# Kernel tuning notes

Measured on AMD Instinct MI355X. Metric: run time of the kernel, lower is better.

Reference implementation:

```python
import jax, jax.numpy as jnp
import numpy as np

CAPACITY_FACTOR = 1.0
MIN_CAPACITY = 4


def setup_inputs() -> dict:
    key = jax.random.key(0)
    ks = jax.random.split(key, 4)
    B, S, D, E, F = 4, 2048, 1024, 16, 4096
    hidden_states = jax.random.normal(ks[0], (B, S, D), dtype=jnp.float32)
    wg = jax.random.normal(ks[1], (D, E), dtype=jnp.float32) * 0.02
    w1 = jax.random.normal(ks[2], (E, D, F), dtype=jnp.float32) * (1.0 / np.sqrt(D))
    b1 = jnp.zeros((E, F), dtype=jnp.float32)
    w2 = jax.random.normal(ks[3], (E, F, D), dtype=jnp.float32) * (1.0 / np.sqrt(F))
    b2 = jnp.zeros((E, D), dtype=jnp.float32)
    return {"hidden_states": hidden_states, "wg": wg, "w1": w1, "b1": b1, "w2": w2, "b2": b2}


def reference(hidden_states, wg, w1, b1, w2, b2):
    B, S, D = hidden_states.shape
    x = hidden_states.reshape(-1, D)                      # [T, D] tokens
    T = x.shape[0]
    E = wg.shape[1]
    capacity = max(int(np.ceil(T / E * CAPACITY_FACTOR)), MIN_CAPACITY)  # static

    # ---- TopKGate (k=1, no noise, no RTS) ----
    logits = x @ wg                                       # [T, E]
    gates = jax.nn.softmax(logits, axis=-1)
    idx1 = jnp.argmax(gates, axis=1)                      # [T]
    mask1 = jax.nn.one_hot(idx1, E, dtype=gates.dtype)    # [T, E]
    exp_counts = jnp.sum(mask1, axis=0).astype(jnp.int32) # per-expert token counts

    # load-balancing aux loss
    me = jnp.mean(gates, axis=0)
    ce = jnp.mean(mask1, axis=0)
    l_aux = jnp.sum(me * ce) * E

    # slot assignment within each expert, drop overflow tokens
    locations1 = jnp.cumsum(mask1, axis=0) - 1.0          # [T, E]
    mask1 = mask1 * (locations1 < capacity).astype(gates.dtype)
    locations1_s = jnp.sum(locations1 * mask1, axis=1).astype(jnp.int32)  # [T]
    gates1 = gates * mask1                                # [T, E] gate prob of kept assignment

    loc_oh = jax.nn.one_hot(locations1_s, capacity, dtype=gates.dtype)    # [T, C]
    combine = jnp.einsum('te,tc->tec', gates1, loc_oh)    # [T, E, C]
    dispatch = (combine > 0).astype(x.dtype)              # [T, E, C]

    # ---- dispatch -> grouped expert FFN -> combine ----
    disp = jnp.einsum('tec,td->ecd', dispatch, x)         # [E, C, D]
    h = jax.nn.gelu(jnp.einsum('ecd,edf->ecf', disp, w1) + b1[:, None, :])
    eo = jnp.einsum('ecf,efd->ecd', h, w2) + b2[:, None, :]  # [E, C, D]
    out = jnp.einsum('tec,ecd->td', combine, eo).reshape(B, S, D)
    return out, l_aux, exp_counts
```

## Files before the change

### kernel.cpp

```cpp
#include <hip/hip_runtime.h>

typedef unsigned short u16;
typedef unsigned int   u32;
typedef unsigned long long u64;
typedef __attribute__((ext_vector_type(8))) __bf16 bf16x8;
typedef __attribute__((ext_vector_type(4))) float  f32x4;

#define TOK 8192
#define DIM 1024
#define NE  16
#define NF  4096
#define CAP 512

__device__ __forceinline__ u16 f2bf(float f) {
    u32 u = __float_as_uint(f);
    u32 r = (u + 0x7FFFu + ((u >> 16) & 1u)) >> 16;
    return (u16)r;
}

__device__ __forceinline__ float gelu_tanh(float x) {
    float u = 0.7978845608028654f * (x + 0.044715f * x * x * x);
    float t = __expf(-2.f * fabsf(u));
    float th = (1.f - t) / (1.f + t);
    th = (u < 0.f) ? -th : th;
    return 0.5f * x * (1.f + th);
}

__device__ __forceinline__ void gld16(const void* g, void* l) {
    __builtin_amdgcn_global_load_lds(
        (const __attribute__((address_space(1))) void*)g,
        (__attribute__((address_space(3))) void*)l, 16, 0, 0);
}

__global__ void moe_init(float* me_sums) {
    if (threadIdx.x < NE) me_sums[threadIdx.x] = 0.f;
}

__global__ void moe_wgT(const float* __restrict__ wg, float* __restrict__ wgT) {
    int i = blockIdx.x * 256 + threadIdx.x;
    int d = i >> 4, e = i & 15;
    wgT[(size_t)e * DIM + d] = wg[i];
}

__global__ void moe_gate(const float* __restrict__ x, const float* __restrict__ wgT,
                         int* __restrict__ eidx, float* __restrict__ gp,
                         float* __restrict__ me_sums) {
    __shared__ float lme[NE];
    const int tid = threadIdx.x;
    if (tid < NE) lme[tid] = 0.f;
    __syncthreads();
    const int tok = blockIdx.x * 16 + (tid >> 4);
    const int e   = tid & 15;
    const float4* xp = (const float4*)(x + (size_t)tok * DIM);
    const float4* wp = (const float4*)(wgT + (size_t)e * DIM);
    float acc = 0.f;
#pragma unroll 4
    for (int i = 0; i < DIM / 4; ++i) {
        float4 a = xp[i], b = wp[i];
        acc = fmaf(a.x, b.x, acc); acc = fmaf(a.y, b.y, acc);
        acc = fmaf(a.z, b.z, acc); acc = fmaf(a.w, b.w, acc);
    }
    float mx = acc;
    for (int off = 8; off; off >>= 1) mx = fmaxf(mx, __shfl_xor(mx, off, 16));
    float ex = __expf(acc - mx);
    float sum = ex;
    for (int off = 8; off; off >>= 1) sum += __shfl_xor(sum, off, 16);
    float p = ex / sum;
    atomicAdd(&lme[e], p);
    float bv = acc; int bi = e;
    for (int off = 8; off; off >>= 1) {
        float ov = __shfl_xor(bv, off, 16);
        int   oi = __shfl_xor(bi, off, 16);
        if (ov > bv || (ov == bv && oi < bi)) { bv = ov; bi = oi; }
    }
    float pw = __shfl(p, bi, 16);
    if (e == 0) { eidx[tok] = bi; gp[tok] = pw; }
    __syncthreads();
    if (tid < 16) atomicAdd(&me_sums[tid], lme[tid]);
}

__global__ void moe_scan(const int* __restrict__ eidx, const float* __restrict__ me_sums,
                         int* __restrict__ slot, int* __restrict__ tos,
                         float* __restrict__ tail ) {
    __shared__ int wcnt[16][16];
    __shared__ int base[16];
    const int tid = threadIdx.x, wid = tid >> 6, lane = tid & 63;
    if (tid < 16) base[tid] = 0;
    for (int i = tid; i < NE * CAP; i += 1024) tos[i] = -1;
    __syncthreads();
    const u64 below = ((u64)1 << lane) - 1;
    for (int chunk = 0; chunk < TOK / 1024; ++chunk) {
        int t = chunk * 1024 + tid;
        int e = eidx[t];
        int rank = 0;
#pragma unroll
        for (int ex = 0; ex < 16; ++ex) {
            u64 m = __ballot(e == ex);
            if (e == ex)    rank = __popcll(m & below);
            if (lane == ex) wcnt[wid][ex] = __popcll(m);
        }
        __syncthreads();
        int pre = base[e];
        for (int w = 0; w < wid; ++w) pre += wcnt[w][e];
        int s = pre + rank;
        slot[t] = s;
        if (s < CAP) tos[e * CAP + s] = t;
        __syncthreads();
        if (tid < 16) {
            int tot = 0;
            for (int w = 0; w < 16; ++w) tot += wcnt[w][tid];
            base[tid] += tot;
        }
        __syncthreads();
    }
    if (tid == 0) {
        float laux = 0.f;
        for (int e2 = 0; e2 < 16; ++e2) {
            float me = me_sums[e2] / (float)TOK;
            float ce = (float)base[e2] / (float)TOK;
            laux += me * ce;
        }
        tail[0] = laux * (float)NE;
    }
    if (tid < 16) tail[1 + tid] = (float)base[tid];
}

__global__ void moe_gather(const float* __restrict__ x, const int* __restrict__ tos,
                           u16* __restrict__ Xg) {
    const int s = blockIdx.x, tid = threadIdx.x;
    const int t = tos[s];
    float4 v = make_float4(0.f, 0.f, 0.f, 0.f);
    if (t >= 0) v = *(const float4*)(x + (size_t)t * DIM + tid * 4);
    u32 lo = (u32)f2bf(v.x) | ((u32)f2bf(v.y) << 16);
    u32 hi = (u32)f2bf(v.z) | ((u32)f2bf(v.w) << 16);
    *(uint2*)(Xg + (size_t)s * DIM + tid * 4) = make_uint2(lo, hi);
}

__global__ void moe_zero_dropped(const int* __restrict__ slot, float* __restrict__ out) {
    const int t = blockIdx.x;
    if (slot[t] < CAP) return;
    *(float4*)(out + (size_t)t * DIM + threadIdx.x * 4) = make_float4(0.f, 0.f, 0.f, 0.f);
}

__global__ void moe_convT(const float* __restrict__ src, u16* __restrict__ dst,
                          int R, int C) {
    __shared__ float tile[64][65];
    int b = blockIdx.x;
    const int tilesC = C >> 6, tilesR = R >> 6;
    int tc = b % tilesC; b /= tilesC;
    int tr = b % tilesR; int e = b / tilesR;
    const float* S = src + ((size_t)e * R + tr * 64) * C + tc * 64;
    const int tid = threadIdx.x;
    const int rr = tid >> 4, cc = (tid & 15) * 4;
#pragma unroll
    for (int i = 0; i < 4; ++i) {
        float4 v = *(const float4*)(S + (size_t)(rr + i * 16) * C + cc);
        tile[rr + i * 16][cc + 0] = v.x; tile[rr + i * 16][cc + 1] = v.y;
        tile[rr + i * 16][cc + 2] = v.z; tile[rr + i * 16][cc + 3] = v.w;
    }
    __syncthreads();
    const int c = tid >> 2, r0 = (tid & 3) * 16;
    u16 tmp[16];
#pragma unroll
    for (int k = 0; k < 16; ++k) tmp[k] = f2bf(tile[r0 + k][c]);
    u16* D = dst + ((size_t)e * C + tc * 64 + c) * R + tr * 64 + r0;
    uint4 w0 = make_uint4((u32)tmp[0] | ((u32)tmp[1] << 16), (u32)tmp[2] | ((u32)tmp[3] << 16),
                          (u32)tmp[4] | ((u32)tmp[5] << 16), (u32)tmp[6] | ((u32)tmp[7] << 16));
    uint4 w1 = make_uint4((u32)tmp[8] | ((u32)tmp[9] << 16), (u32)tmp[10] | ((u32)tmp[11] << 16),
                          (u32)tmp[12] | ((u32)tmp[13] << 16), (u32)tmp[14] | ((u32)tmp[15] << 16));
    *(uint4*)(D) = w0;
    *(uint4*)(D + 8) = w1;
}

__global__ __launch_bounds__(512, 2) void moe_gemm1(const u16* __restrict__ Xg,
                                                    const u16* __restrict__ W1t,
                                                    const float* __restrict__ b1,
                                                    u16* __restrict__ H) {
    __shared__ alignas(16) u16 Als[3][8192];
    __shared__ alignas(16) u16 Bls[3][8192];
    const int tid = threadIdx.x, wave = tid >> 6, lane = tid & 63;
    const int flat = blockIdx.x;
    const int xcd  = flat & 7;
    const int slot = flat >> 3;
    const int e    = xcd * 2 + (slot >> 5);
    const int tile = slot & 31;
    const int bm   = tile & 1;
    const int bn   = tile >> 1;
    const int r4   = lane >> 2;
    const int gch  = (lane & 3) ^ ((lane >> 3) & 3);
    const u16* aSrc = Xg + (size_t)(e * 512 + bm * 256 + wave * 16 + r4) * DIM + gch * 8;
    const u16* bSrc = W1t + (size_t)e * NF * DIM
                    + (size_t)(bn * 256 + wave * 16 + r4) * DIM + gch * 8;
    const int wm = wave & 1, wn = wave >> 1;
    const int fr = lane & 15, fq = lane >> 4;
    const int rdoff = fr * 32 + (fq ^ ((fr >> 1) & 3)) * 8;

    f32x4 acc[2][4][4] = {};

#define STAGE1(P, T) do { \
        const int ko = (T) * 32; \
        u16* ad = &Als[P][wave * 512]; \
        u16* bd = &Bls[P][wave * 512]; \
        gld16(aSrc + ko, ad); \
        gld16(aSrc + 128 * DIM + ko, ad + 4096); \
        gld16(bSrc + ko, bd); \
        gld16(bSrc + 128 * DIM + ko, bd + 4096); } while (0)

    const int NT = DIM / 32;
    STAGE1(0, 0);
    STAGE1(1, 1);
    int c = 0;
    for (int t = 0; t < NT; ++t) {
        if (t < NT - 1) { asm volatile("s_waitcnt vmcnt(4)" ::: "memory"); }
        else            { asm volatile("s_waitcnt vmcnt(0)" ::: "memory"); }
        __builtin_amdgcn_sched_barrier(0);
        __builtin_amdgcn_s_barrier();
        __builtin_amdgcn_sched_barrier(0);
        const u16* Ab = &Als[c][0];
        const u16* Bb = &Bls[c][0];
        bf16x8 bF[4], aF[4];
#pragma unroll
        for (int j = 0; j < 4; ++j)
            bF[j] = *(const bf16x8*)(const void*)(Bb + (wn * 64 + j * 16) * 32 + rdoff);
#pragma unroll
        for (int i = 0; i < 4; ++i)
            aF[i] = *(const bf16x8*)(const void*)(Ab + (wm * 128 + i * 16) * 32 + rdoff);
        if (t + 2 < NT) {
            const int p = (c + 2 >= 3) ? (c - 1) : (c + 2);
            STAGE1(p, t + 2);
        }
        __builtin_amdgcn_sched_barrier(0);
        __builtin_amdgcn_s_setprio(1);
#pragma unroll
        for (int i = 0; i < 4; ++i)
#pragma unroll
            for (int j = 0; j < 4; ++j)
                acc[0][i][j] = __builtin_amdgcn_mfma_f32_16x16x32_bf16(aF[i], bF[j], acc[0][i][j], 0, 0, 0);
        __builtin_amdgcn_s_setprio(0);
#pragma unroll
        for (int i = 0; i < 4; ++i)
            aF[i] = *(const bf16x8*)(const void*)(Ab + (wm * 128 + 64 + i * 16) * 32 + rdoff);
        __builtin_amdgcn_s_setprio(1);
#pragma unroll
        for (int i = 0; i < 4; ++i)
#pragma unroll
            for (int j = 0; j < 4; ++j)
                acc[1][i][j] = __builtin_amdgcn_mfma_f32_16x16x32_bf16(aF[i], bF[j], acc[1][i][j], 0, 0, 0);
        __builtin_amdgcn_s_setprio(0);
        c = (c == 2) ? 0 : c + 1;
    }
#undef STAGE1

    const int mBase = e * 512 + bm * 256 + wm * 128;
    const int nBase = bn * 256 + wn * 64;
#pragma unroll
    for (int j = 0; j < 4; ++j) {
        const int f = nBase + j * 16 + fr;
        const float bias = b1[e * NF + f];
#pragma unroll
        for (int q = 0; q < 2; ++q)
#pragma unroll
            for (int i = 0; i < 4; ++i) {
                const int m0 = mBase + q * 64 + i * 16 + fq * 4;
#pragma unroll
                for (int r = 0; r < 4; ++r) {
                    float v = acc[q][i][j][r] + bias;
                    H[(size_t)(m0 + r) * NF + f] = f2bf(gelu_tanh(v));
                }
            }
    }
}

__global__ __launch_bounds__(512, 2) void moe_gemm2(const u16* __restrict__ H,
                                                    const u16* __restrict__ W2t,
                                                    const float* __restrict__ b2,
                                                    const int* __restrict__ tos,
                                                    const float* __restrict__ gp,
                                                    float* __restrict__ out) {
    __shared__ alignas(16) u16 Als[3][8192];
    __shared__ alignas(16) u16 Bls[3][4096];
    const int tid = threadIdx.x, wave = tid >> 6, lane = tid & 63;
    const int flat = blockIdx.x;
    const int xcd  = flat & 7;
    const int slot = flat >> 3;
    const int e    = xcd * 2 + (slot >> 4);
    const int tile = slot & 15;
    const int bm   = tile & 1;
    const int bn   = tile >> 1;
    const int r4   = lane >> 2;
    const int gch  = (lane & 3) ^ ((lane >> 3) & 3);
    const u16* aSrc = H + (size_t)(e * 512 + bm * 256 + wave * 16 + r4) * NF + gch * 8;
    const u16* bSrc = W2t + (size_t)e * DIM * NF
                    + (size_t)(bn * 128 + wave * 16 + r4) * NF + gch * 8;
    const int wm = wave & 1, wn = wave >> 1;
    const int fr = lane & 15, fq = lane >> 4;
    const int rdoff = fr * 32 + (fq ^ ((fr >> 1) & 3)) * 8;

    f32x4 acc[2][4][2] = {};

#define STAGE2(P, T) do { \
        const int ko = (T) * 32; \
        u16* ad = &Als[P][wave * 512]; \
        u16* bd = &Bls[P][wave * 512]; \
        gld16(aSrc + ko, ad); \
        gld16(aSrc + (size_t)128 * NF + ko, ad + 4096); \
        gld16(bSrc + ko, bd); } while (0)

    const int NT = NF / 32;
    STAGE2(0, 0);
    STAGE2(1, 1);
    int c = 0;
    for (int t = 0; t < NT; ++t) {
        if (t < NT - 1) { asm volatile("s_waitcnt vmcnt(3)" ::: "memory"); }
        else            { asm volatile("s_waitcnt vmcnt(0)" ::: "memory"); }
        __builtin_amdgcn_sched_barrier(0);
        __builtin_amdgcn_s_barrier();
        __builtin_amdgcn_sched_barrier(0);
        const u16* Ab = &Als[c][0];
        const u16* Bb = &Bls[c][0];
        bf16x8 bF[2], aF[4];
#pragma unroll
        for (int j = 0; j < 2; ++j)
            bF[j] = *(const bf16x8*)(const void*)(Bb + (wn * 32 + j * 16) * 32 + rdoff);
#pragma unroll
        for (int i = 0; i < 4; ++i)
            aF[i] = *(const bf16x8*)(const void*)(Ab + (wm * 128 + i * 16) * 32 + rdoff);
        if (t + 2 < NT) {
            const int p = (c + 2 >= 3) ? (c - 1) : (c + 2);
            STAGE2(p, t + 2);
        }
        __builtin_amdgcn_sched_barrier(0);
        __builtin_amdgcn_s_setprio(1);
#pragma unroll
        for (int i = 0; i < 4; ++i)
#pragma unroll
            for (int j = 0; j < 2; ++j)
                acc[0][i][j] = __builtin_amdgcn_mfma_f32_16x16x32_bf16(aF[i], bF[j], acc[0][i][j], 0, 0, 0);
        __builtin_amdgcn_s_setprio(0);
#pragma unroll
        for (int i = 0; i < 4; ++i)
            aF[i] = *(const bf16x8*)(const void*)(Ab + (wm * 128 + 64 + i * 16) * 32 + rdoff);
        __builtin_amdgcn_s_setprio(1);
#pragma unroll
        for (int i = 0; i < 4; ++i)
#pragma unroll
            for (int j = 0; j < 2; ++j)
                acc[1][i][j] = __builtin_amdgcn_mfma_f32_16x16x32_bf16(aF[i], bF[j], acc[1][i][j], 0, 0, 0);
        __builtin_amdgcn_s_setprio(0);
        c = (c == 2) ? 0 : c + 1;
    }
#undef STAGE2

    const int mBase = e * 512 + bm * 256 + wm * 128;
    const int nBase = bn * 128 + wn * 32;
#pragma unroll
    for (int q = 0; q < 2; ++q)
#pragma unroll
        for (int i = 0; i < 4; ++i) {
#pragma unroll
            for (int r = 0; r < 4; ++r) {
                const int m = mBase + q * 64 + i * 16 + fq * 4 + r;
                const int t = tos[m];
                if (t < 0) continue;
                const float g = gp[t];
#pragma unroll
                for (int j = 0; j < 2; ++j) {
                    const int d = nBase + j * 16 + fr;
                    out[(size_t)t * DIM + d] = g * (acc[q][i][j][r] + b2[e * DIM + d]);
                }
            }
        }
}

extern "C" void kernel_launch(void* const* d_in, const int* in_sizes, int n_in,
                              void* d_out, int out_size, void* d_ws, size_t ws_size,
                              hipStream_t stream) {
    const float* x  = (const float*)d_in[0];
    const float* wg = (const float*)d_in[1];
    const float* w1 = (const float*)d_in[2];
    const float* b1 = (const float*)d_in[3];
    const float* w2 = (const float*)d_in[4];
    const float* b2 = (const float*)d_in[5];
    float* out = (float*)d_out;

    char* ws = (char*)d_ws;
    const size_t WBF_OFF = 0;
    const size_t XG_OFF  = WBF_OFF + (size_t)NE * NF * DIM * 2;
    const size_t H_OFF   = XG_OFF + (size_t)TOK * DIM * 2;
    const size_t SM_OFF  = H_OFF + (size_t)TOK * NF * 2;
    u16* Wbf = (u16*)(ws + WBF_OFF);
    u16* Xg  = (u16*)(ws + XG_OFF);
    u16* H   = (u16*)(ws + H_OFF);
    int*   eidx = (int*)(ws + SM_OFF);
    float* gp   = (float*)(ws + SM_OFF + 32768);
    int*   slot = (int*)(ws + SM_OFF + 65536);
    int*   tos  = (int*)(ws + SM_OFF + 98304);
    float* me   = (float*)(ws + SM_OFF + 131072);
    float* wgT  = (float*)(ws + SM_OFF + 131072 + 128);

    float* tail = out + (size_t)TOK * DIM;

    moe_init<<<1, 64, 0, stream>>>(me);
    moe_wgT<<<64, 256, 0, stream>>>(wg, wgT);
    moe_gate<<<TOK / 16, 256, 0, stream>>>(x, wgT, eidx, gp, me);
    moe_scan<<<1, 1024, 0, stream>>>(eidx, me, slot, tos, tail);
    moe_gather<<<NE * CAP, 256, 0, stream>>>(x, tos, Xg);
    moe_zero_dropped<<<TOK, 256, 0, stream>>>(slot, out);
    moe_convT<<<NE * (DIM / 64) * (NF / 64), 256, 0, stream>>>(w1, Wbf, DIM, NF);
    moe_gemm1<<<512, 512, 0, stream>>>(Xg, Wbf, b1, H);
    moe_convT<<<NE * (NF / 64) * (DIM / 64), 256, 0, stream>>>(w2, Wbf, NF, DIM);
    moe_gemm2<<<256, 512, 0, stream>>>(H, Wbf, b2, tos, gp, out);
}
```

Before: 929.4 us.

## Deepen expert GEMM pipelines to four LDS stages and split A/B prefetch

Both grouped expert GEMMs move from a triple-buffered to a quad-buffered LDS pipeline, prefetching three K-tiles ahead with adjusted vmcnt waits. The A and B tile prefetches are split across the two MFMA half-steps, with an extra barrier and explicit lgkmcnt waits in between. The goal is to hide more global-load latency and spread load issue across the loop. In exchange, LDS per block grows; for the second GEMM this likely drops residency from two blocks per CU to one, and the extra barrier per iteration adds sync cost.

```diff
diff --git a/kernel.cpp b/kernel.cpp
--- a/kernel.cpp
+++ b/kernel.cpp
@@ -176,8 +176,8 @@
                                                     const u16* __restrict__ W1t,
                                                     const float* __restrict__ b1,
                                                     u16* __restrict__ H) {
-    __shared__ alignas(16) u16 Als[3][8192];
-    __shared__ alignas(16) u16 Bls[3][8192];
+    __shared__ alignas(16) u16 Als[4][8192];
+    __shared__ alignas(16) u16 Bls[4][8192];
     const int tid = threadIdx.x, wave = tid >> 6, lane = tid & 63;
     const int flat = blockIdx.x;
     const int xcd  = flat & 7;
@@ -197,22 +197,21 @@
 
     f32x4 acc[2][4][4] = {};
 
-#define STAGE1(P, T) do { \
-        const int ko = (T) * 32; \
-        u16* ad = &Als[P][wave * 512]; \
-        u16* bd = &Bls[P][wave * 512]; \
-        gld16(aSrc + ko, ad); \
-        gld16(aSrc + 128 * DIM + ko, ad + 4096); \
-        gld16(bSrc + ko, bd); \
-        gld16(bSrc + 128 * DIM + ko, bd + 4096); } while (0)
+#define STG1A(P, T) do { const int ko = (T) * 32; u16* ad = &Als[P][wave * 512]; \
+        gld16(aSrc + ko, ad); gld16(aSrc + 128 * DIM + ko, ad + 4096); } while (0)
+#define STG1B(P, T) do { const int ko = (T) * 32; u16* bd = &Bls[P][wave * 512]; \
+        gld16(bSrc + ko, bd); gld16(bSrc + 128 * DIM + ko, bd + 4096); } while (0)
 
     const int NT = DIM / 32;
-    STAGE1(0, 0);
-    STAGE1(1, 1);
-    int c = 0;
+    STG1A(0, 0); STG1B(0, 0);
+    STG1A(1, 1); STG1B(1, 1);
+    STG1A(2, 2); STG1B(2, 2);
     for (int t = 0; t < NT; ++t) {
-        if (t < NT - 1) { asm volatile("s_waitcnt vmcnt(4)" ::: "memory"); }
-        else            { asm volatile("s_waitcnt vmcnt(0)" ::: "memory"); }
+        const int c = t & 3;
+        const int rem = NT - 1 - t;
+        if (rem >= 2)      asm volatile("s_waitcnt vmcnt(8)" ::: "memory");
+        else if (rem == 1) asm volatile("s_waitcnt vmcnt(4)" ::: "memory");
+        else               asm volatile("s_waitcnt vmcnt(0)" ::: "memory");
         __builtin_amdgcn_sched_barrier(0);
         __builtin_amdgcn_s_barrier();
         __builtin_amdgcn_sched_barrier(0);
@@ -225,10 +224,9 @@
 #pragma unroll
         for (int i = 0; i < 4; ++i)
             aF[i] = *(const bf16x8*)(const void*)(Ab + (wm * 128 + i * 16) * 32 + rdoff);
-        if (t + 2 < NT) {
-            const int p = (c + 2 >= 3) ? (c - 1) : (c + 2);
-            STAGE1(p, t + 2);
-        }
+        if (t + 3 < NT) STG1A((c + 3) & 3, t + 3);
+        __builtin_amdgcn_sched_barrier(0);
+        asm volatile("s_waitcnt lgkmcnt(0)" ::: "memory");
         __builtin_amdgcn_sched_barrier(0);
         __builtin_amdgcn_s_setprio(1);
 #pragma unroll
@@ -237,9 +235,16 @@
             for (int j = 0; j < 4; ++j)
                 acc[0][i][j] = __builtin_amdgcn_mfma_f32_16x16x32_bf16(aF[i], bF[j], acc[0][i][j], 0, 0, 0);
         __builtin_amdgcn_s_setprio(0);
+        __builtin_amdgcn_sched_barrier(0);
+        __builtin_amdgcn_s_barrier();
+        __builtin_amdgcn_sched_barrier(0);
 #pragma unroll
         for (int i = 0; i < 4; ++i)
             aF[i] = *(const bf16x8*)(const void*)(Ab + (wm * 128 + 64 + i * 16) * 32 + rdoff);
+        if (t + 3 < NT) STG1B((c + 3) & 3, t + 3);
+        __builtin_amdgcn_sched_barrier(0);
+        asm volatile("s_waitcnt lgkmcnt(0)" ::: "memory");
+        __builtin_amdgcn_sched_barrier(0);
         __builtin_amdgcn_s_setprio(1);
 #pragma unroll
         for (int i = 0; i < 4; ++i)
@@ -247,9 +252,9 @@
             for (int j = 0; j < 4; ++j)
                 acc[1][i][j] = __builtin_amdgcn_mfma_f32_16x16x32_bf16(aF[i], bF[j], acc[1][i][j], 0, 0, 0);
         __builtin_amdgcn_s_setprio(0);
-        c = (c == 2) ? 0 : c + 1;
-    }
-#undef STAGE1
+    }
+#undef STG1A
+#undef STG1B
 
     const int mBase = e * 512 + bm * 256 + wm * 128;
     const int nBase = bn * 256 + wn * 64;
@@ -277,8 +282,8 @@
                                                     const int* __restrict__ tos,
                                                     const float* __restrict__ gp,
                                                     float* __restrict__ out) {
-    __shared__ alignas(16) u16 Als[3][8192];
-    __shared__ alignas(16) u16 Bls[3][4096];
+    __shared__ alignas(16) u16 Als[4][8192];
+    __shared__ alignas(16) u16 Bls[4][4096];
     const int tid = threadIdx.x, wave = tid >> 6, lane = tid & 63;
     const int flat = blockIdx.x;
     const int xcd  = flat & 7;
@@ -298,21 +303,21 @@
 
     f32x4 acc[2][4][2] = {};
 
-#define STAGE2(P, T) do { \
-        const int ko = (T) * 32; \
-        u16* ad = &Als[P][wave * 512]; \
-        u16* bd = &Bls[P][wave * 512]; \
-        gld16(aSrc + ko, ad); \
-        gld16(aSrc + (size_t)128 * NF + ko, ad + 4096); \
+#define STG2A(P, T) do { const int ko = (T) * 32; u16* ad = &Als[P][wave * 512]; \
+        gld16(aSrc + ko, ad); gld16(aSrc + (size_t)128 * NF + ko, ad + 4096); } while (0)
+#define STG2B(P, T) do { const int ko = (T) * 32; u16* bd = &Bls[P][wave * 512]; \
         gld16(bSrc + ko, bd); } while (0)
 
     const int NT = NF / 32;
-    STAGE2(0, 0);
-    STAGE2(1, 1);
-    int c = 0;
+    STG2A(0, 0); STG2B(0, 0);
+    STG2A(1, 1); STG2B(1, 1);
+    STG2A(2, 2); STG2B(2, 2);
     for (int t = 0; t < NT; ++t) {
-        if (t < NT - 1) { asm volatile("s_waitcnt vmcnt(3)" ::: "memory"); }
-        else            { asm volatile("s_waitcnt vmcnt(0)" ::: "memory"); }
+        const int c = t & 3;
+        const int rem = NT - 1 - t;
+        if (rem >= 2)      asm volatile("s_waitcnt vmcnt(6)" ::: "memory");
+        else if (rem == 1) asm volatile("s_waitcnt vmcnt(3)" ::: "memory");
+        else               asm volatile("s_waitcnt vmcnt(0)" ::: "memory");
         __builtin_amdgcn_sched_barrier(0);
         __builtin_amdgcn_s_barrier();
         __builtin_amdgcn_sched_barrier(0);
@@ -325,10 +330,9 @@
 #pragma unroll
         for (int i = 0; i < 4; ++i)
             aF[i] = *(const bf16x8*)(const void*)(Ab + (wm * 128 + i * 16) * 32 + rdoff);
-        if (t + 2 < NT) {
-            const int p = (c + 2 >= 3) ? (c - 1) : (c + 2);
-            STAGE2(p, t + 2);
-        }
+        if (t + 3 < NT) STG2A((c + 3) & 3, t + 3);
+        __builtin_amdgcn_sched_barrier(0);
+        asm volatile("s_waitcnt lgkmcnt(0)" ::: "memory");
         __builtin_amdgcn_sched_barrier(0);
         __builtin_amdgcn_s_setprio(1);
 #pragma unroll
@@ -337,9 +341,16 @@
             for (int j = 0; j < 2; ++j)
                 acc[0][i][j] = __builtin_amdgcn_mfma_f32_16x16x32_bf16(aF[i], bF[j], acc[0][i][j], 0, 0, 0);
         __builtin_amdgcn_s_setprio(0);
+        __builtin_amdgcn_sched_barrier(0);
+        __builtin_amdgcn_s_barrier();
+        __builtin_amdgcn_sched_barrier(0);
 #pragma unroll
         for (int i = 0; i < 4; ++i)
             aF[i] = *(const bf16x8*)(const void*)(Ab + (wm * 128 + 64 + i * 16) * 32 + rdoff);
+        if (t + 3 < NT) STG2B((c + 3) & 3, t + 3);
+        __builtin_amdgcn_sched_barrier(0);
+        asm volatile("s_waitcnt lgkmcnt(0)" ::: "memory");
+        __builtin_amdgcn_sched_barrier(0);
         __builtin_amdgcn_s_setprio(1);
 #pragma unroll
         for (int i = 0; i < 4; ++i)
@@ -347,9 +358,9 @@
             for (int j = 0; j < 2; ++j)
                 acc[1][i][j] = __builtin_amdgcn_mfma_f32_16x16x32_bf16(aF[i], bF[j], acc[1][i][j], 0, 0, 0);
         __builtin_amdgcn_s_setprio(0);
-        c = (c == 2) ? 0 : c + 1;
-    }
-#undef STAGE2
+    }
+#undef STG2A
+#undef STG2B
 
     const int mBase = e * 512 + bm * 256 + wm * 128;
     const int nBase = bn * 128 + wn * 32;
```

New measurement: 917.5 us. Within noise of the previous version (-1.3%).
